# Performance work log

Hardware: AMD Instinct MI355X
Metric: run time of the kernel (lower is better)

The kernel has to match this reference:

```python
import jax, jax.numpy as jnp
import numpy as np

EPS = 1e-15


def _trace(t):
    return jnp.einsum('bii->b', t)


def _ortho_loss(ss, k):
    n = jnp.linalg.norm(ss, axis=(-1, -2), keepdims=True)
    diff = ss / n - jnp.eye(k, dtype=ss.dtype) / np.float32(np.sqrt(k))
    return jnp.mean(jnp.linalg.norm(diff, axis=(-1, -2)))


def _mincut_terms(s, adj):
    out_adj = jnp.einsum('bnk,bnm,bml->bkl', s, adj, s)
    d_flat = adj.sum(-1)  # degrees [B,N]
    num = _trace(out_adj)
    den = _trace(jnp.einsum('bnk,bn,bnl->bkl', s, d_flat, s)) + EPS
    return out_adj, num, den, d_flat


def dense_mincut_rewiring(x, adj, s, mask):
    k = s.shape[-1]  # 2
    m = mask[..., None].astype(x.dtype)
    s = jax.nn.softmax(s, axis=-1) * m
    _, num, den, _ = _mincut_terms(s, adj)
    mincut_loss = -jnp.mean(num / den)
    ortho_loss = _ortho_loss(jnp.einsum('bnk,bnl->bkl', s, s), k)
    # laplacian derivative of spectral gap wrt A_uv: (f_u - f_v)^2, f = soft bipartition
    f = s[..., 0]
    dlam = (f[:, :, None] - f[:, None, :]) ** 2
    return adj * (1.0 - dlam), mincut_loss, ortho_loss


def dense_CT_rewiring(x, adj, s, mask):
    k = s.shape[-1]
    m = mask[..., None].astype(x.dtype)
    s = jax.nn.softmax(s, axis=-1) * m
    d_flat = adj.sum(-1)
    sds = _trace(jnp.einsum('bnk,bn,bnl->bkl', s, d_flat, s))
    sas = _trace(jnp.einsum('bnk,bnm,bml->bkl', s, adj, s))
    den = _trace(jnp.einsum('bnk,bnl->bkl', s, s)) + EPS
    ct_loss = jnp.mean((sds - sas) / den)  # tr(Z^T L Z) / tr(Z^T Z)
    ortho_loss = _ortho_loss(jnp.einsum('bnk,bnl->bkl', s, s), k)
    # pairwise CT distances ||z_u - z_v|| / vol(G), sparsified by A
    sq = (s * s).sum(-1)
    d2 = sq[:, :, None] + sq[:, None, :] - 2.0 * jnp.einsum('bnk,bmk->bnm', s, s)
    ct_dist = jnp.sqrt(jnp.maximum(d2, 0.0) + 1e-12)
    vol = d_flat.sum(-1)
    new_adj = (ct_dist / (vol[:, None, None] + EPS)) * adj
    return new_adj, ct_loss, ortho_loss


def dense_mincut_pool(x, adj, s, mask):
    k = s.shape[-1]
    m = mask[..., None].astype(x.dtype)
    s = jax.nn.softmax(s, axis=-1) * m
    x = x * m
    out = jnp.einsum('bnk,bnf->bkf', s, x)
    out_adj, num, den, _ = _mincut_terms(s, adj)
    mincut_loss = -jnp.mean(num / den)
    ortho_loss = _ortho_loss(jnp.einsum('bnk,bnl->bkl', s, s), k)
    out_adj = out_adj * (1.0 - jnp.eye(k, dtype=adj.dtype))  # zero diagonal
    d = jnp.sqrt(out_adj.sum(-1)) + EPS  # [B,k]
    out_adj = out_adj / d[:, None, :] / d[:, :, None]
    return out, out_adj, mincut_loss, ortho_loss


def _dgc(x, adj, w_rel, b_rel, w_root):
    # DenseGraphConv(aggr='add'): lin_rel(A @ x) + lin_root(x)
    return jnp.matmul(adj, x) @ w_rel + b_rel + x @ w_root


def setup_inputs() -> dict:
    B, N, IN, H, KC, OUT, KMC = 16, 1024, 128, 32, 32, 10, 16
    keys = iter(jax.random.split(jax.random.key(0), 48))

    def lin(fin, fout):
        lim = float(1.0 / np.sqrt(fin))
        return (jax.random.uniform(next(keys), (fin, fout), jnp.float32, -lim, lim),
                jax.random.uniform(next(keys), (fout,), jnp.float32, -lim, lim))

    x = jax.random.normal(next(keys), (B, N, IN), jnp.float32)
    u = jax.random.uniform(next(keys), (B, N, N), jnp.float32)
    a = (u < 0.0156).astype(jnp.float32)  # avg degree ~16
    adj = jnp.maximum(a, jnp.swapaxes(a, 1, 2)) * (1.0 - jnp.eye(N, dtype=jnp.float32))
    mask = jnp.ones((B, N), dtype=bool)
    W1, b1 = lin(IN, H)
    Wrw, brw = lin(H, 2)
    Wg_rel, bg = lin(H, H); Wg_root, _ = lin(H, H)
    Wmcg, bmcg = lin(H, KMC)
    W2g_rel, b2g = lin(H, H); W2g_root, _ = lin(H, H)
    Wct, bct = lin(H, KC)
    Wc_rel, bc = lin(H, H); Wc_root, _ = lin(H, H)
    Wmcc, bmcc = lin(H, KMC)
    Wcat, bcat = lin(2 * H, H)
    W2, b2 = lin(H, H)
    W3, b3 = lin(H, OUT)
    return dict(x=x, adj=adj, mask=mask, W1=W1, b1=b1, Wrw=Wrw, brw=brw,
                Wg_rel=Wg_rel, bg=bg, Wg_root=Wg_root, Wmcg=Wmcg, bmcg=bmcg,
                W2g_rel=W2g_rel, b2g=b2g, W2g_root=W2g_root, Wct=Wct, bct=bct,
                Wc_rel=Wc_rel, bc=bc, Wc_root=Wc_root, Wmcc=Wmcc, bmcc=bmcc,
                Wcat=Wcat, bcat=bcat, W2=W2, b2=b2, W3=W3, b3=b3)


def reference(x, adj, mask, W1, b1, Wrw, brw, Wg_rel, bg, Wg_root, Wmcg, bmcg,
              W2g_rel, b2g, W2g_root, Wct, bct, Wc_rel, bc, Wc_root, Wmcc, bmcc,
              Wcat, bcat, W2, b2, W3, b3):
    x = x @ W1 + b1
    # GAP branch
    adj_gap, mc_rw, ol_rw = dense_mincut_rewiring(x, adj, x @ Wrw + brw, mask)
    x_gap = _dgc(x, adj_gap, Wg_rel, bg, Wg_root)
    x_gap, adj_gap, mc1, ol1 = dense_mincut_pool(x_gap, adj_gap, x_gap @ Wmcg + bmcg, mask)
    x_gap = _dgc(x_gap, adj_gap, W2g_rel, b2g, W2g_root)
    # CT branch
    adj_ct, ct_loss, ol_ct = dense_CT_rewiring(x, adj, x @ Wct + bct, mask)
    x_ct = _dgc(x, adj_ct, Wc_rel, bc, Wc_root)
    x_ct, adj_ct, mc2, ol2 = dense_mincut_pool(x_ct, adj_ct, x_ct @ Wmcc + bmcc, mask)
    x_ct = _dgc(x_ct, adj_ct, W2g_rel, b2g, W2g_root)  # source reuses self.conv2gap here
    h = jax.nn.relu(jnp.concatenate([x_gap, x_ct], axis=2) @ Wcat + bcat).sum(axis=1)
    h = jax.nn.relu(h @ W2 + b2)
    logits = h @ W3 + b3
    main_loss = mc_rw + ct_loss + mc1 + mc2
    ortho_loss = ol_rw + ol_ct + ol1 + ol2
    return (jax.nn.log_softmax(logits, axis=-1), main_loss, ortho_loss)
```

## Files before the change

### kernel.cpp

```cpp
#include <hip/hip_runtime.h>
#include <math.h>

#define BB   16
#define NNODE 1024
#define INF_ 128
#define HH   32
#define KMC  16
#define CAP  128
#define EPS15 1e-15f

#define OFF_X      0
#define OFF_SRW    524288
#define OFF_SQCT   557056
#define OFF_SCT    573440
#define OFF_D      1097728
#define OFF_NUMRW  1114112
#define OFF_SAS    1130496
#define OFF_DGAP   1146880
#define OFF_DCT    1163264
#define OFF_YGAP   1179648
#define OFF_YCT    1703936
#define OFF_XGAP   2228224
#define OFF_XCT    2752512
#define OFF_S2G    3276800
#define OFF_S2C    3538944
#define OFF_TG     3801088
#define OFF_TC     4063232
#define OFF_FROB   4325376
#define OFF_VOL    4325888
#define OFF_MCRW   4325904
#define OFF_CTB    4325920
#define OFF_OLRW   4325936
#define OFF_OLCT   4325952
#define OFF_MC1    4325968
#define OFF_MC2    4325984
#define OFF_OL1    4326000
#define OFF_OL2    4326016
#define OFF_OUTG   4326032
#define OFF_OUTC   4334224
#define OFF_G2G    4342416
#define OFF_G2C    4346512
#define OFF_OAG    4350608
#define OFF_OAC    4354704

__device__ __forceinline__ float wave_sum(float v) {
#pragma unroll
  for (int off = 32; off >= 1; off >>= 1) v += __shfl_xor(v, off, 64);
  return v;
}

__device__ __forceinline__ float blk_sum(float v, float* sred, int tid) {
  v = wave_sum(v);
  __syncthreads();
  if ((tid & 63) == 0) sred[tid >> 6] = v;
  __syncthreads();
  return sred[0] + sred[1] + sred[2] + sred[3];
}

__global__ __launch_bounds__(256) void k_prep(
    const float* __restrict__ x, const float* __restrict__ W1, const float* __restrict__ b1,
    const float* __restrict__ Wrw, const float* __restrict__ brw,
    const float* __restrict__ Wct, const float* __restrict__ bct,
    float* __restrict__ ws)
{
  __shared__ float sW1[INF_*HH];
  __shared__ float sWct[HH*HH];
  __shared__ float sWrw[HH*2];
  __shared__ float sb1[HH], sbct[HH], sbrw[2];
  __shared__ float sx[8*INF_];
  __shared__ float sX[8*HH];
  int tid = threadIdx.x;
  for (int i = tid; i < INF_*HH; i += 256) sW1[i] = W1[i];
  for (int i = tid; i < HH*HH; i += 256) sWct[i] = Wct[i];
  if (tid < HH*2) sWrw[tid] = Wrw[tid];
  if (tid < HH) { sb1[tid] = b1[tid]; sbct[tid] = bct[tid]; }
  if (tid < 2) sbrw[tid] = brw[tid];
  size_t row0 = (size_t)blockIdx.x * 8;
  ((float4*)sx)[tid] = ((const float4*)(x + row0 * INF_))[tid];
  __syncthreads();
  int r = tid >> 5, h = tid & 31;
  float acc = sb1[h];
#pragma unroll 8
  for (int k = 0; k < INF_; k++) acc += sx[r*INF_ + k] * sW1[k*HH + h];
  size_t row = row0 + r;
  ws[OFF_X + row*HH + h] = acc;
  sX[r*HH + h] = acc;
  __syncthreads();
  float sraw = sbct[h];
#pragma unroll
  for (int k = 0; k < HH; k++) sraw += sX[r*HH + k] * sWct[k*HH + h];
  float mx = sraw;
#pragma unroll
  for (int off = 16; off >= 1; off >>= 1) mx = fmaxf(mx, __shfl_xor(mx, off, 32));
  float e = __expf(sraw - mx);
  float sum = e;
#pragma unroll
  for (int off = 16; off >= 1; off >>= 1) sum += __shfl_xor(sum, off, 32);
  float sv = e / sum;
  ws[OFF_SCT + row*HH + h] = sv;
  float sq = sv * sv;
#pragma unroll
  for (int off = 16; off >= 1; off >>= 1) sq += __shfl_xor(sq, off, 32);
  float xv = sX[r*HH + h];
  float t0 = xv * sWrw[h*2 + 0];
  float t1 = xv * sWrw[h*2 + 1];
#pragma unroll
  for (int off = 16; off >= 1; off >>= 1) { t0 += __shfl_xor(t0, off, 32); t1 += __shfl_xor(t1, off, 32); }
  if (h == 0) {
    ws[OFF_SQCT + row] = sq;
    float r0 = t0 + sbrw[0], r1 = t1 + sbrw[1];
    float m2 = fmaxf(r0, r1);
    float e0 = __expf(r0 - m2), e1 = __expf(r1 - m2);
    float inv = 1.0f / (e0 + e1);
    ((float2*)(ws + OFF_SRW))[row] = make_float2(e0*inv, e1*inv);
  }
}

__global__ __launch_bounds__(256) void k_pass1(const float* __restrict__ adj, float* __restrict__ ws)
{
  __shared__ int   s_m[4][CAP];
  __shared__ float s_a[4][CAP];
  __shared__ float s_wg[4][CAP];
  __shared__ float s_wc[4][CAP];
  const float* X = ws + OFF_X;
  const float2* srw = (const float2*)(ws + OFF_SRW);
  const float* sqct = ws + OFF_SQCT;
  const float* sct = ws + OFF_SCT;
  int tid = threadIdx.x;
  int w = tid >> 6, lane = tid & 63;
  int row = blockIdx.x * 4 + w;
  int b = row >> 10;
  const float4* arow4 = (const float4*)(adj + (size_t)row * NNODE);
  const float4* cn4 = (const float4*)(sct + (size_t)row * HH);
  float4 c[8];
#pragma unroll
  for (int i = 0; i < 8; i++) c[i] = cn4[i];
  float2 srwn = srw[row];
  float f_n = srwn.x;
  float sq_n = sqct[row];
  float dpart = 0.f;
  int base = 0;
#pragma unroll
  for (int it = 0; it < 4; it++) {
    float4 a4 = arow4[it*64 + lane];
    int m0 = it*256 + lane*4;
    float av[4] = {a4.x, a4.y, a4.z, a4.w};
#pragma unroll
    for (int j = 0; j < 4; j++) {
      float a = av[j];
      dpart += a;
      unsigned long long mk = __ballot(a != 0.0f);
      if (a != 0.0f) {
        int pos = base + (int)__popcll(mk & ((1ull << lane) - 1ull));
        if (pos < CAP) { s_m[w][pos] = m0 + j; s_a[w][pos] = a; }
      }
      base += (int)__popcll(mk);
    }
  }
  int nnz = base < CAP ? base : CAP;
  float d_n = wave_sum(dpart);
  __syncthreads();
  float numrw_p = 0.f, sas_p = 0.f, dg_p = 0.f, dc_p = 0.f;
  for (int e = lane; e < nnz; e += 64) {
    int m = s_m[w][e];
    float a = s_a[w][e];
    const float4* cm4 = (const float4*)(sct + ((size_t)b*NNODE + m) * HH);
    float dot = 0.f;
#pragma unroll
    for (int i = 0; i < 8; i++) {
      float4 d4 = cm4[i];
      dot += c[i].x*d4.x + c[i].y*d4.y + c[i].z*d4.z + c[i].w*d4.w;
    }
    float2 srwm = srw[b*NNODE + m];
    numrw_p += a * (srwn.x*srwm.x + srwn.y*srwm.y);
    float df = f_n - srwm.x;
    float wg = a * (1.0f - df*df);
    float d2 = sq_n + sqct[b*NNODE + m] - 2.0f*dot;
    float wc = a * sqrtf(fmaxf(d2, 0.0f) + 1e-12f);
    sas_p += a * dot;
    dg_p += wg;
    dc_p += wc;
    s_wg[w][e] = wg;
    s_wc[w][e] = wc;
  }
  float numrw = wave_sum(numrw_p);
  float sas = wave_sum(sas_p);
  float dgp = wave_sum(dg_p);
  float dcp = wave_sum(dc_p);
  if (lane == 0) {
    ws[OFF_D + row] = d_n;
    ws[OFF_NUMRW + row] = numrw;
    ws[OFF_SAS + row] = sas;
    ws[OFF_DGAP + row] = dgp;
    ws[OFF_DCT + row] = dcp;
  }
  __syncthreads();
  int h = lane & 31, half = lane >> 5;
  float yg = 0.f, yc = 0.f;
  for (int e = half; e < nnz; e += 2) {
    int m = s_m[w][e];
    float wg = s_wg[w][e], wc = s_wc[w][e];
    float Xv = X[((size_t)b*NNODE + m)*HH + h];
    yg += wg * Xv;
    yc += wc * Xv;
  }
  yg += __shfl_xor(yg, 32, 64);
  yc += __shfl_xor(yc, 32, 64);
  if (half == 0) {
    ws[OFF_YGAP + (size_t)row*HH + h] = yg;
    ws[OFF_YCT + (size_t)row*HH + h] = yc;
  }
}

__global__ __launch_bounds__(256) void k_gramfrob(float* __restrict__ ws)
{
  int blk = blockIdx.x;
  int b = blk >> 5, i = blk & 31;
  const float* sct = ws + OFF_SCT + (size_t)b*NNODE*HH;
  int tid = threadIdx.x;
  int j = tid & 31, seg = tid >> 5;
  float acc = 0.f;
  for (int n = seg*128; n < seg*128 + 128; n++)
    acc += sct[n*HH + i] * sct[n*HH + j];
  __shared__ float sp[8][32];
  sp[seg][j] = acc;
  __syncthreads();
  if (tid < 32) {
    float g = 0.f;
#pragma unroll
    for (int s = 0; s < 8; s++) g += sp[s][tid];
    float p = g * g;
#pragma unroll
    for (int off = 16; off >= 1; off >>= 1) p += __shfl_xor(p, off, 32);
    if (tid == 0) ws[OFF_FROB + blk] = p;
  }
}

__global__ __launch_bounds__(256) void k_batch1(float* __restrict__ ws)
{
  __shared__ float sred[4];
  int b = blockIdx.x, tid = threadIdx.x;
  for (int i = tid; i < 2048; i += 256) ws[OFF_OUTG + b*2048 + i] = 0.f;
  size_t base = (size_t)b * NNODE;
  const float2* srw = (const float2*)(ws + OFF_SRW);
  float vol_p=0, denrw_p=0, num_p=0, sds_p=0, sas_p=0, denct_p=0, g00_p=0, g01_p=0, g11_p=0;
  for (int n = tid; n < NNODE; n += 256) {
    float d = ws[OFF_D + base + n];
    float2 s = srw[base + n];
    float sq = ws[OFF_SQCT + base + n];
    vol_p += d;
    denrw_p += d * (s.x*s.x + s.y*s.y);
    num_p += ws[OFF_NUMRW + base + n];
    sds_p += d * sq;
    sas_p += ws[OFF_SAS + base + n];
    denct_p += sq;
    g00_p += s.x*s.x; g01_p += s.x*s.y; g11_p += s.y*s.y;
  }
  float frob_p = (tid < 32) ? ws[OFF_FROB + b*32 + tid] : 0.f;
  float vol = blk_sum(vol_p, sred, tid);
  float denrw = blk_sum(denrw_p, sred, tid);
  float num = blk_sum(num_p, sred, tid);
  float sds = blk_sum(sds_p, sred, tid);
  float sas = blk_sum(sas_p, sred, tid);
  float denct = blk_sum(denct_p, sred, tid);
  float g00 = blk_sum(g00_p, sred, tid);
  float g01 = blk_sum(g01_p, sred, tid);
  float g11 = blk_sum(g11_p, sred, tid);
  float frob2 = blk_sum(frob_p, sred, tid);
  if (tid == 0) {
    ws[OFF_VOL + b] = vol;
    ws[OFF_MCRW + b] = -num / (denrw + EPS15);
    ws[OFF_CTB + b] = (sds - sas) / (denct + EPS15);
    float nrw = sqrtf(g00*g00 + 2.f*g01*g01 + g11*g11);
    ws[OFF_OLRW + b] = sqrtf(fmaxf(2.f - 2.f*(g00 + g11)/(nrw*1.41421356237f), 0.f));
    float nct = sqrtf(frob2);
    ws[OFF_OLCT + b] = sqrtf(fmaxf(2.f - 2.f*denct/(nct*5.65685424949f), 0.f));
  }
}

__global__ __launch_bounds__(256) void k_feat(
    const float* __restrict__ Wg_rel, const float* __restrict__ bg, const float* __restrict__ Wg_root,
    const float* __restrict__ Wc_rel, const float* __restrict__ bc, const float* __restrict__ Wc_root,
    const float* __restrict__ Wmcg, const float* __restrict__ bmcg,
    const float* __restrict__ Wmcc, const float* __restrict__ bmcc,
    float* __restrict__ ws)
{
  __shared__ float sWgrel[HH*HH], sWgroot[HH*HH], sWcrel[HH*HH], sWcroot[HH*HH];
  __shared__ float sWmcg[HH*KMC], sWmcc[HH*KMC];
  __shared__ float sbg[HH], sbc[HH], sbmcg[KMC], sbmcc[KMC];
  __shared__ float syg[8*HH], syc[8*HH], sXl[8*HH], sxg[8*HH], sxc[8*HH];
  int tid = threadIdx.x;
  for (int i = tid; i < HH*HH; i += 256) {
    sWgrel[i] = Wg_rel[i]; sWgroot[i] = Wg_root[i];
    sWcrel[i] = Wc_rel[i]; sWcroot[i] = Wc_root[i];
  }
  for (int i = tid; i < HH*KMC; i += 256) { sWmcg[i] = Wmcg[i]; sWmcc[i] = Wmcc[i]; }
  if (tid < HH) { sbg[tid] = bg[tid]; sbc[tid] = bc[tid]; }
  if (tid < KMC) { sbmcg[tid] = bmcg[tid]; sbmcc[tid] = bmcc[tid]; }
  size_t row0 = (size_t)blockIdx.x * 8;
  int b = (int)(row0 >> 10);
  syg[tid] = ws[OFF_YGAP + row0*HH + tid];
  syc[tid] = ws[OFF_YCT + row0*HH + tid];
  sXl[tid] = ws[OFF_X + row0*HH + tid];
  __syncthreads();
  float ivol = 1.0f / (ws[OFF_VOL + b] + EPS15);
  int r = tid >> 5, h = tid & 31;
  float accg = 0.f, accg2 = 0.f, accc = 0.f, accc2 = 0.f;
#pragma unroll
  for (int k = 0; k < HH; k++) {
    float ygv = syg[r*HH + k], Xv = sXl[r*HH + k], ycv = syc[r*HH + k];
    accg  += ygv * sWgrel[k*HH + h];
    accg2 += Xv  * sWgroot[k*HH + h];
    accc  += ycv * sWcrel[k*HH + h];
    accc2 += Xv  * sWcroot[k*HH + h];
  }
  float xgv = sbg[h] + accg + accg2;
  float xcv = sbc[h] + ivol*accc + accc2;
  size_t row = row0 + r;
  ws[OFF_XGAP + row*HH + h] = xgv;
  ws[OFF_XCT + row*HH + h] = xcv;
  sxg[r*HH + h] = xgv;
  sxc[r*HH + h] = xcv;
  __syncthreads();
  int j = h & 15, halfsel = h >> 4;
  const float* sin_ = halfsel ? sxc : sxg;
  const float* sw = halfsel ? sWmcc : sWmcg;
  float raw = halfsel ? sbmcc[j] : sbmcg[j];
#pragma unroll
  for (int k = 0; k < HH; k++) raw += sin_[r*HH + k] * sw[k*KMC + j];
  float mx = raw;
#pragma unroll
  for (int off = 8; off >= 1; off >>= 1) mx = fmaxf(mx, __shfl_xor(mx, off, 16));
  float e = __expf(raw - mx);
  float sum = e;
#pragma unroll
  for (int off = 8; off >= 1; off >>= 1) sum += __shfl_xor(sum, off, 16);
  float sv = e / sum;
  if (halfsel == 0) ws[OFF_S2G + row*KMC + j] = sv;
  else              ws[OFF_S2C + row*KMC + j] = sv;
}

__global__ __launch_bounds__(256) void k_pass2(const float* __restrict__ adj, float* __restrict__ ws)
{
  __shared__ int   s_m[4][CAP];
  __shared__ float s_wg[4][CAP];
  __shared__ float s_wc[4][CAP];
  const float* sct = ws + OFF_SCT;
  const float* sqct = ws + OFF_SQCT;
  const float2* srw = (const float2*)(ws + OFF_SRW);
  int tid = threadIdx.x;
  int w = tid >> 6, lane = tid & 63;
  int row = blockIdx.x * 4 + w;
  int b = row >> 10;
  const float4* arow4 = (const float4*)(adj + (size_t)row * NNODE);
  const float4* cn4 = (const float4*)(sct + (size_t)row * HH);
  float4 c[8];
#pragma unroll
  for (int i = 0; i < 8; i++) c[i] = cn4[i];
  float f_n = srw[row].x;
  float sq_n = sqct[row];
  int base = 0;
#pragma unroll
  for (int it = 0; it < 4; it++) {
    float4 a4 = arow4[it*64 + lane];
    int m0 = it*256 + lane*4;
    float av[4] = {a4.x, a4.y, a4.z, a4.w};
#pragma unroll
    for (int j = 0; j < 4; j++) {
      float a = av[j];
      unsigned long long mk = __ballot(a != 0.0f);
      if (a != 0.0f) {
        int pos = base + (int)__popcll(mk & ((1ull << lane) - 1ull));
        if (pos < CAP) { s_m[w][pos] = m0 + j; s_wg[w][pos] = a; }
      }
      base += (int)__popcll(mk);
    }
  }
  int nnz = base < CAP ? base : CAP;
  __syncthreads();
  for (int e = lane; e < nnz; e += 64) {
    int m = s_m[w][e];
    float a = s_wg[w][e];
    const float4* cm4 = (const float4*)(sct + ((size_t)b*NNODE + m) * HH);
    float dot = 0.f;
#pragma unroll
    for (int i = 0; i < 8; i++) {
      float4 d4 = cm4[i];
      dot += c[i].x*d4.x + c[i].y*d4.y + c[i].z*d4.z + c[i].w*d4.w;
    }
    float df = f_n - srw[b*NNODE + m].x;
    float wg = a * (1.0f - df*df);
    float d2 = sq_n + sqct[b*NNODE + m] - 2.0f*dot;
    float wc = a * sqrtf(fmaxf(d2, 0.0f) + 1e-12f);
    s_wg[w][e] = wg;
    s_wc[w][e] = wc;
  }
  __syncthreads();
  int h16 = lane & 15, which = (lane >> 4) & 1, half = lane >> 5;
  const float* sp = ws + (which ? OFF_S2C : OFF_S2G);
  float acc = 0.f;
  for (int e = half; e < nnz; e += 2) {
    int m = s_m[w][e];
    float wv = which ? s_wc[w][e] : s_wg[w][e];
    acc += wv * sp[((size_t)b*NNODE + m)*KMC + h16];
  }
  acc += __shfl_xor(acc, 32, 64);
  if (half == 0) {
    float* tp = ws + (which ? OFF_TC : OFF_TG);
    tp[(size_t)row*KMC + h16] = acc;
  }
}

__global__ __launch_bounds__(256) void k_red2(float* __restrict__ ws)
{
  __shared__ float sg[64*16], sc[64*16], stg[64*16], stc[64*16];
  __shared__ float sxg[64*32], sxc[64*32];
  int b = blockIdx.x >> 4, chunk = blockIdx.x & 15;
  int tid = threadIdx.x;
  size_t n0 = (size_t)b * NNODE + chunk * 64;
  const float* pG  = ws + OFF_S2G  + n0 * KMC;
  const float* pC  = ws + OFF_S2C  + n0 * KMC;
  const float* pTG = ws + OFF_TG   + n0 * KMC;
  const float* pTC = ws + OFF_TC   + n0 * KMC;
  const float* pXG = ws + OFF_XGAP + n0 * HH;
  const float* pXC = ws + OFF_XCT  + n0 * HH;
#pragma unroll
  for (int i = 0; i < 4; i++) {
    sg [tid + i*256] = pG [tid + i*256];
    sc [tid + i*256] = pC [tid + i*256];
    stg[tid + i*256] = pTG[tid + i*256];
    stc[tid + i*256] = pTC[tid + i*256];
  }
#pragma unroll
  for (int i = 0; i < 8; i++) {
    sxg[tid + i*256] = pXG[tid + i*256];
    sxc[tid + i*256] = pXC[tid + i*256];
  }
  __syncthreads();
  int k0 = tid >> 5, h0 = tid & 31;
  float og0 = 0.f, og1 = 0.f, oc0 = 0.f, oc1 = 0.f;
#pragma unroll 8
  for (int r = 0; r < 64; r++) {
    float xgv = sxg[r*32 + h0], xcv = sxc[r*32 + h0];
    og0 += sg[r*16 + k0]     * xgv;
    og1 += sg[r*16 + k0 + 8] * xgv;
    oc0 += sc[r*16 + k0]     * xcv;
    oc1 += sc[r*16 + k0 + 8] * xcv;
  }
  atomicAdd(&ws[OFF_OUTG + b*512 + k0*32 + h0],       og0);
  atomicAdd(&ws[OFF_OUTG + b*512 + (k0+8)*32 + h0],   og1);
  atomicAdd(&ws[OFF_OUTC + b*512 + k0*32 + h0],       oc0);
  atomicAdd(&ws[OFF_OUTC + b*512 + (k0+8)*32 + h0],   oc1);
  int k = tid >> 4, l = tid & 15;
  float gg = 0.f, gc = 0.f, ag = 0.f, ac = 0.f;
#pragma unroll 8
  for (int r = 0; r < 64; r++) {
    float sgk = sg[r*16 + k], sck = sc[r*16 + k];
    gg += sgk * sg [r*16 + l];
    gc += sck * sc [r*16 + l];
    ag += sgk * stg[r*16 + l];
    ac += sck * stc[r*16 + l];
  }
  atomicAdd(&ws[OFF_G2G + b*256 + tid], gg);
  atomicAdd(&ws[OFF_G2C + b*256 + tid], gc);
  atomicAdd(&ws[OFF_OAG + b*256 + tid], ag);
  atomicAdd(&ws[OFF_OAC + b*256 + tid], ac);
}

__global__ __launch_bounds__(256) void k_batch2(
    const float* __restrict__ W2g_rel, const float* __restrict__ b2g, const float* __restrict__ W2g_root,
    const float* __restrict__ Wcat, const float* __restrict__ bcat,
    const float* __restrict__ W2, const float* __restrict__ b2,
    const float* __restrict__ W3, const float* __restrict__ b3,
    float* __restrict__ out, float* __restrict__ ws)
{
  __shared__ float sOAg[256], sOAc[256], sOutg[512], sOutc[512];
  __shared__ float sW2grel[1024], sW2groot[1024], sWcat[2048], sW2l[1024];
  __shared__ float sPg[512], sPc[512], sXg2[512], sXc2[512], sHt[512];
  __shared__ float sHs[32], sH2[32], sLg[16], sScal[2];
  __shared__ float sdkg[16], sdkc[16];
  __shared__ float sred[4];
  int b = blockIdx.x, tid = threadIdx.x;
  sOAg[tid] = ws[OFF_OAG + b*256 + tid];
  sOAc[tid] = ws[OFF_OAC + b*256 + tid];
  sOutg[tid] = ws[OFF_OUTG + b*512 + tid];
  sOutg[tid + 256] = ws[OFF_OUTG + b*512 + tid + 256];
  sOutc[tid] = ws[OFF_OUTC + b*512 + tid];
  sOutc[tid + 256] = ws[OFF_OUTC + b*512 + tid + 256];
  for (int i = tid; i < 1024; i += 256) { sW2grel[i] = W2g_rel[i]; sW2groot[i] = W2g_root[i]; sW2l[i] = W2[i]; }
  for (int i = tid; i < 2048; i += 256) sWcat[i] = Wcat[i];
  size_t base = (size_t)b * NNODE;
  float den1_p = 0, den2_p = 0, trg_p = 0, trc_p = 0;
  for (int n = tid; n < NNODE; n += 256) {
    float dg = ws[OFF_DGAP + base + n], dc = ws[OFF_DCT + base + n];
    const float* pg = ws + OFF_S2G + (base + n)*KMC;
    const float* pc = ws + OFF_S2C + (base + n)*KMC;
    float ng = 0.f, nc = 0.f;
#pragma unroll
    for (int j = 0; j < KMC; j++) { ng += pg[j]*pg[j]; nc += pc[j]*pc[j]; }
    den1_p += dg * ng; den2_p += dc * nc; trg_p += ng; trc_p += nc;
  }
  float den1 = blk_sum(den1_p, sred, tid);
  float den2u = blk_sum(den2_p, sred, tid);
  float trg = blk_sum(trg_p, sred, tid);
  float trc = blk_sum(trc_p, sred, tid);
  float gv = ws[OFF_G2G + b*256 + tid];
  float cv = ws[OFF_G2C + b*256 + tid];
  float frobg2 = blk_sum(gv*gv, sred, tid);
  float frobc2 = blk_sum(cv*cv, sred, tid);
  float t1_p = (tid < 16) ? sOAg[tid*17] : 0.f;
  float t2_p = (tid < 16) ? sOAc[tid*17] : 0.f;
  float num1 = blk_sum(t1_p, sred, tid);
  float num2u = blk_sum(t2_p, sred, tid);
  float vol = ws[OFF_VOL + b];
  float ivol = 1.0f / (vol + EPS15);
  if (tid == 0) {
    ws[OFF_MC1 + b] = -num1 / (den1 + EPS15);
    ws[OFF_MC2 + b] = -(num2u*ivol) / (den2u*ivol + EPS15);
    ws[OFF_OL1 + b] = sqrtf(fmaxf(2.f - 2.f*trg/(sqrtf(frobg2)*4.f), 0.f));
    ws[OFF_OL2 + b] = sqrtf(fmaxf(2.f - 2.f*trc/(sqrtf(frobc2)*4.f), 0.f));
  }
  sOAc[tid] *= ivol;
  __syncthreads();
  if (tid < 16) { sOAg[tid*17] = 0.f; sOAc[tid*17] = 0.f; }
  __syncthreads();
  if (tid < 16) {
    float rg = 0.f, rc = 0.f;
#pragma unroll
    for (int l = 0; l < 16; l++) { rg += sOAg[tid*16 + l]; rc += sOAc[tid*16 + l]; }
    sdkg[tid] = sqrtf(rg) + EPS15;
    sdkc[tid] = sqrtf(rc) + EPS15;
  }
  __syncthreads();
  { int k = tid >> 4, l = tid & 15;
    sOAg[tid] /= (sdkg[k]*sdkg[l]);
    sOAc[tid] /= (sdkc[k]*sdkc[l]); }
  __syncthreads();
  { int k = tid >> 5, h = tid & 31;
    float p0 = 0, p1 = 0, q0 = 0, q1 = 0;
#pragma unroll
    for (int l = 0; l < 16; l++) {
      p0 += sOAg[k*16 + l] * sOutg[l*32 + h];
      p1 += sOAg[(k+8)*16 + l] * sOutg[l*32 + h];
      q0 += sOAc[k*16 + l] * sOutc[l*32 + h];
      q1 += sOAc[(k+8)*16 + l] * sOutc[l*32 + h];
    }
    sPg[k*32 + h] = p0; sPg[(k+8)*32 + h] = p1;
    sPc[k*32 + h] = q0; sPc[(k+8)*32 + h] = q1;
  }
  __syncthreads();
  { int k = tid >> 5, h = tid & 31;
    float bb2 = b2g[h];
    float a0 = bb2, a1 = bb2, c0 = bb2, c1 = bb2;
#pragma unroll
    for (int q = 0; q < 32; q++) {
      float wr = sW2grel[q*32 + h], wo = sW2groot[q*32 + h];
      a0 += sPg[k*32 + q]*wr + sOutg[k*32 + q]*wo;
      a1 += sPg[(k+8)*32 + q]*wr + sOutg[(k+8)*32 + q]*wo;
      c0 += sPc[k*32 + q]*wr + sOutc[k*32 + q]*wo;
      c1 += sPc[(k+8)*32 + q]*wr + sOutc[(k+8)*32 + q]*wo;
    }
    sXg2[k*32 + h] = a0; sXg2[(k+8)*32 + h] = a1;
    sXc2[k*32 + h] = c0; sXc2[(k+8)*32 + h] = c1;
  }
  __syncthreads();
  { int k = tid >> 5, h = tid & 31;
    float bb = bcat[h];
    float t0 = bb, t1 = bb;
#pragma unroll
    for (int q = 0; q < 32; q++) {
      float w1v = sWcat[q*32 + h], w2v = sWcat[(q+32)*32 + h];
      t0 += sXg2[k*32 + q]*w1v + sXc2[k*32 + q]*w2v;
      t1 += sXg2[(k+8)*32 + q]*w1v + sXc2[(k+8)*32 + q]*w2v;
    }
    sHt[k*32 + h] = fmaxf(t0, 0.f);
    sHt[(k+8)*32 + h] = fmaxf(t1, 0.f);
  }
  __syncthreads();
  if (tid < 32) {
    float s = 0.f;
#pragma unroll
    for (int k = 0; k < 16; k++) s += sHt[k*32 + tid];
    sHs[tid] = s;
  }
  __syncthreads();
  if (tid < 32) {
    float a = b2[tid];
#pragma unroll
    for (int q = 0; q < 32; q++) a += sHs[q]*sW2l[q*32 + tid];
    sH2[tid] = fmaxf(a, 0.f);
  }
  __syncthreads();
  if (tid < 10) {
    float a = b3[tid];
#pragma unroll
    for (int q = 0; q < 32; q++) a += sH2[q]*W3[q*10 + tid];
    sLg[tid] = a;
  }
  __syncthreads();
  if (tid == 0) {
    float m = sLg[0];
    for (int o = 1; o < 10; o++) m = fmaxf(m, sLg[o]);
    float se = 0.f;
    for (int o = 0; o < 10; o++) se += __expf(sLg[o] - m);
    sScal[0] = m; sScal[1] = logf(se);
  }
  __syncthreads();
  if (tid < 10) out[b*10 + tid] = sLg[tid] - sScal[0] - sScal[1];
}

__global__ void k_loss(float* __restrict__ out, const float* __restrict__ ws)
{
  int t = threadIdx.x;
  float vm = 0.f, vo = 0.f;
  if (t < BB) {
    vm = ws[OFF_MCRW + t] + ws[OFF_CTB + t] + ws[OFF_MC1 + t] + ws[OFF_MC2 + t];
    vo = ws[OFF_OLRW + t] + ws[OFF_OLCT + t] + ws[OFF_OL1 + t] + ws[OFF_OL2 + t];
  }
  vm = wave_sum(vm);
  vo = wave_sum(vo);
  if (t == 0) { out[160] = vm / 16.f; out[161] = vo / 16.f; }
}

extern "C" void kernel_launch(void* const* d_in, const int* in_sizes, int n_in,
                              void* d_out, int out_size, void* d_ws, size_t ws_size,
                              hipStream_t stream)
{
  const float* x       = (const float*)d_in[0];
  const float* adj     = (const float*)d_in[1];
  const float* W1      = (const float*)d_in[3];
  const float* b1      = (const float*)d_in[4];
  const float* Wrw     = (const float*)d_in[5];
  const float* brw     = (const float*)d_in[6];
  const float* Wg_rel  = (const float*)d_in[7];
  const float* bg      = (const float*)d_in[8];
  const float* Wg_root = (const float*)d_in[9];
  const float* Wmcg    = (const float*)d_in[10];
  const float* bmcg    = (const float*)d_in[11];
  const float* W2g_rel = (const float*)d_in[12];
  const float* b2g     = (const float*)d_in[13];
  const float* W2g_root= (const float*)d_in[14];
  const float* Wct     = (const float*)d_in[15];
  const float* bct     = (const float*)d_in[16];
  const float* Wc_rel  = (const float*)d_in[17];
  const float* bc      = (const float*)d_in[18];
  const float* Wc_root = (const float*)d_in[19];
  const float* Wmcc    = (const float*)d_in[20];
  const float* bmcc    = (const float*)d_in[21];
  const float* Wcat    = (const float*)d_in[22];
  const float* bcat    = (const float*)d_in[23];
  const float* W2      = (const float*)d_in[24];
  const float* b2      = (const float*)d_in[25];
  const float* W3      = (const float*)d_in[26];
  const float* b3      = (const float*)d_in[27];
  float* out = (float*)d_out;
  float* ws  = (float*)d_ws;

  k_prep<<<dim3(2048), dim3(256), 0, stream>>>(x, W1, b1, Wrw, brw, Wct, bct, ws);
  k_pass1<<<dim3(4096), dim3(256), 0, stream>>>(adj, ws);
  k_gramfrob<<<dim3(512), dim3(256), 0, stream>>>(ws);
  k_batch1<<<dim3(16), dim3(256), 0, stream>>>(ws);
  k_feat<<<dim3(2048), dim3(256), 0, stream>>>(Wg_rel, bg, Wg_root, Wc_rel, bc, Wc_root,
                                               Wmcg, bmcg, Wmcc, bmcc, ws);
  k_pass2<<<dim3(4096), dim3(256), 0, stream>>>(adj, ws);
  k_red2<<<dim3(256), dim3(256), 0, stream>>>(ws);
  k_batch2<<<dim3(16), dim3(256), 0, stream>>>(W2g_rel, b2g, W2g_root, Wcat, bcat,
                                               W2, b2, W3, b3, out, ws);
  k_loss<<<dim3(1), dim3(64), 0, stream>>>(out, ws);
}
```

Measured before the change: 292.8 us.

## Cache sparse edge lists from pass1 to skip re-reading adjacency in pass2

Pass1 now writes each row's compacted neighbour indices and the GAP and CT edge weights into workspace. A new k_pass2c kernel consumes these cached lists instead of re-scanning the dense 64MB adjacency matrix and recomputing the weights. Pass1 also hoists its adjacency loads ahead of the loop and gathers X with float2 across four edge lanes. This adds extra workspace writes and depends on the workspace being large enough; otherwise it falls back to the old pass2.

```diff
diff --git a/kernel.cpp b/kernel.cpp
--- a/kernel.cpp
+++ b/kernel.cpp
@@ -42,6 +42,11 @@
 #define OFF_G2C    4346512
 #define OFF_OAG    4350608
 #define OFF_OAC    4354704
+#define OFF_ENNZ   4358800
+#define OFF_EIDX   4375184
+#define OFF_EWG    5423760
+#define OFF_EWC    7520912
+#define WS_NEED    9618064
 
 __device__ __forceinline__ float wave_sum(float v) {
 #pragma unroll
@@ -116,7 +121,8 @@
   }
 }
 
-__global__ __launch_bounds__(256) void k_pass1(const float* __restrict__ adj, float* __restrict__ ws)
+__global__ __launch_bounds__(256) void k_pass1(const float* __restrict__ adj, float* __restrict__ ws,
+                                               int do_cache)
 {
   __shared__ int   s_m[4][CAP];
   __shared__ float s_a[4][CAP];
@@ -132,6 +138,9 @@
   int b = row >> 10;
   const float4* arow4 = (const float4*)(adj + (size_t)row * NNODE);
   const float4* cn4 = (const float4*)(sct + (size_t)row * HH);
+  float4 a4s[4];
+#pragma unroll
+  for (int it = 0; it < 4; it++) a4s[it] = arow4[it*64 + lane];
   float4 c[8];
 #pragma unroll
   for (int i = 0; i < 8; i++) c[i] = cn4[i];
@@ -142,7 +151,7 @@
   int base = 0;
 #pragma unroll
   for (int it = 0; it < 4; it++) {
-    float4 a4 = arow4[it*64 + lane];
+    float4 a4 = a4s[it];
     int m0 = it*256 + lane*4;
     float av[4] = {a4.x, a4.y, a4.z, a4.w};
 #pragma unroll
@@ -182,6 +191,12 @@
     dc_p += wc;
     s_wg[w][e] = wg;
     s_wc[w][e] = wc;
+    if (do_cache) {
+      size_t eo = (size_t)row*CAP + e;
+      ((unsigned short*)(ws + OFF_EIDX))[eo] = (unsigned short)m;
+      ws[OFF_EWG + eo] = wg;
+      ws[OFF_EWC + eo] = wc;
+    }
   }
   float numrw = wave_sum(numrw_p);
   float sas = wave_sum(sas_p);
@@ -193,22 +208,25 @@
     ws[OFF_SAS + row] = sas;
     ws[OFF_DGAP + row] = dgp;
     ws[OFF_DCT + row] = dcp;
-  }
-  __syncthreads();
-  int h = lane & 31, half = lane >> 5;
-  float yg = 0.f, yc = 0.f;
-  for (int e = half; e < nnz; e += 2) {
+    if (do_cache) ((int*)(ws + OFF_ENNZ))[row] = nnz;
+  }
+  __syncthreads();
+  int eoff = lane >> 4, hp = lane & 15;
+  float yg0 = 0.f, yg1 = 0.f, yc0 = 0.f, yc1 = 0.f;
+  for (int e = eoff; e < nnz; e += 4) {
     int m = s_m[w][e];
     float wg = s_wg[w][e], wc = s_wc[w][e];
-    float Xv = X[((size_t)b*NNODE + m)*HH + h];
-    yg += wg * Xv;
-    yc += wc * Xv;
-  }
-  yg += __shfl_xor(yg, 32, 64);
-  yc += __shfl_xor(yc, 32, 64);
-  if (half == 0) {
-    ws[OFF_YGAP + (size_t)row*HH + h] = yg;
-    ws[OFF_YCT + (size_t)row*HH + h] = yc;
+    float2 xv = ((const float2*)(X + ((size_t)b*NNODE + m)*HH))[hp];
+    yg0 += wg*xv.x; yg1 += wg*xv.y;
+    yc0 += wc*xv.x; yc1 += wc*xv.y;
+  }
+  yg0 += __shfl_xor(yg0, 16, 64); yg0 += __shfl_xor(yg0, 32, 64);
+  yg1 += __shfl_xor(yg1, 16, 64); yg1 += __shfl_xor(yg1, 32, 64);
+  yc0 += __shfl_xor(yc0, 16, 64); yc0 += __shfl_xor(yc0, 32, 64);
+  yc1 += __shfl_xor(yc1, 16, 64); yc1 += __shfl_xor(yc1, 32, 64);
+  if (eoff == 0) {
+    ((float2*)(ws + OFF_YGAP + (size_t)row*HH))[hp] = make_float2(yg0, yg1);
+    ((float2*)(ws + OFF_YCT  + (size_t)row*HH))[hp] = make_float2(yc0, yc1);
   }
 }
 
@@ -338,6 +356,34 @@
   float sv = e / sum;
   if (halfsel == 0) ws[OFF_S2G + row*KMC + j] = sv;
   else              ws[OFF_S2C + row*KMC + j] = sv;
+}
+
+__global__ __launch_bounds__(256) void k_pass2c(float* __restrict__ ws)
+{
+  int tid = threadIdx.x;
+  int w = tid >> 6, lane = tid & 63;
+  int row = blockIdx.x * 4 + w;
+  int b = row >> 10;
+  int nnz = ((const int*)(ws + OFF_ENNZ))[row];
+  const unsigned short* eidx = (const unsigned short*)(ws + OFF_EIDX) + (size_t)row*CAP;
+  const float* ewg = ws + OFF_EWG + (size_t)row*CAP;
+  const float* ewc = ws + OFF_EWC + (size_t)row*CAP;
+  const float* S2G = ws + OFF_S2G + (size_t)b*NNODE*KMC;
+  const float* S2C = ws + OFF_S2C + (size_t)b*NNODE*KMC;
+  int eoff = lane >> 4, j = lane & 15;
+  float tg = 0.f, tc = 0.f;
+  for (int e = eoff; e < nnz; e += 4) {
+    int m = eidx[e];
+    float wg = ewg[e], wc = ewc[e];
+    tg += wg * S2G[m*KMC + j];
+    tc += wc * S2C[m*KMC + j];
+  }
+  tg += __shfl_xor(tg, 16, 64); tg += __shfl_xor(tg, 32, 64);
+  tc += __shfl_xor(tc, 16, 64); tc += __shfl_xor(tc, 32, 64);
+  if (eoff == 0) {
+    ws[OFF_TG + (size_t)row*KMC + j] = tg;
+    ws[OFF_TC + (size_t)row*KMC + j] = tc;
+  }
 }
 
 __global__ __launch_bounds__(256) void k_pass2(const float* __restrict__ adj, float* __restrict__ ws)
@@ -655,14 +701,16 @@
   const float* b3      = (const float*)d_in[27];
   float* out = (float*)d_out;
   float* ws  = (float*)d_ws;
+  const int cache = (ws_size >= (size_t)WS_NEED * sizeof(float)) ? 1 : 0;
 
   k_prep<<<dim3(2048), dim3(256), 0, stream>>>(x, W1, b1, Wrw, brw, Wct, bct, ws);
-  k_pass1<<<dim3(4096), dim3(256), 0, stream>>>(adj, ws);
+  k_pass1<<<dim3(4096), dim3(256), 0, stream>>>(adj, ws, cache);
   k_gramfrob<<<dim3(512), dim3(256), 0, stream>>>(ws);
   k_batch1<<<dim3(16), dim3(256), 0, stream>>>(ws);
   k_feat<<<dim3(2048), dim3(256), 0, stream>>>(Wg_rel, bg, Wg_root, Wc_rel, bc, Wc_root,
                                                Wmcg, bmcg, Wmcc, bmcc, ws);
-  k_pass2<<<dim3(4096), dim3(256), 0, stream>>>(adj, ws);
+  if (cache) k_pass2c<<<dim3(4096), dim3(256), 0, stream>>>(ws);
+  else       k_pass2 <<<dim3(4096), dim3(256), 0, stream>>>(adj, ws);
   k_red2<<<dim3(256), dim3(256), 0, stream>>>(ws);
   k_batch2<<<dim3(16), dim3(256), 0, stream>>>(W2g_rel, b2g, W2g_root, Wcat, bcat,
                                                W2, b2, W3, b3, out, ws);
```

Result: faster. 261.9 us (-10.6%).
